# Kernel optimization log

Hardware: AMD Instinct MI355X
Metric: run time of the kernel (lower is better)

## Reference

```python
import jax, jax.numpy as jnp
import numpy as np

BN_EPS = 1e-5
K2 = 9  # 3x3 kernel


def _conv3x3(x, w, b):
    # x: [B,C,H,W], w: [O,C,3,3] -> [B,O,H,W], stride 1, pad 1
    out = jax.lax.conv_general_dilated(
        x, w, window_strides=(1, 1), padding=((1, 1), (1, 1)),
        dimension_numbers=("NCHW", "OIHW", "NCHW"))
    return out + b[None, :, None, None]


def setup_inputs() -> dict:
    key = jax.random.key(0)
    ks = jax.random.split(key, 8)
    B, C, H, W = 8, 256, 64, 64
    O = 256
    x = jax.random.normal(ks[0], (B, C, H, W), dtype=jnp.float32)
    # offset/mask conv: small init so sampled offsets stay near the base grid
    w_off = jax.random.normal(ks[1], (3 * K2, C, 3, 3), dtype=jnp.float32) * 0.01
    b_off = jnp.zeros((3 * K2,), dtype=jnp.float32)
    weight = jax.random.normal(ks[2], (O, C, 3, 3), dtype=jnp.float32) * 0.02
    bias = jnp.zeros((O,), dtype=jnp.float32)
    gamma = jnp.ones((O,), dtype=jnp.float32)
    beta = jnp.zeros((O,), dtype=jnp.float32)
    run_mean = jax.random.normal(ks[3], (O,), dtype=jnp.float32) * 0.1
    run_var = jax.random.uniform(ks[4], (O,), dtype=jnp.float32) + 0.5
    return {"x": x, "w_off": w_off, "b_off": b_off, "weight": weight,
            "bias": bias, "gamma": gamma, "beta": beta,
            "run_mean": run_mean, "run_var": run_var}


def _deform_sample(img, py, px):
    # img: [C,H,W]; py, px: [K2,H,W] sampling coordinates.
    # Bilinear sample with zero padding outside (DCNv2 semantics:
    # out-of-bounds corners contribute zero).
    C, H, W = img.shape
    y0 = jnp.floor(py)
    x0 = jnp.floor(px)
    wy1 = py - y0  # frac weights for the 'high' corner
    wx1 = px - x0

    def gather(yi, xi):
        valid = (yi >= 0) & (yi < H) & (xi >= 0) & (xi < W)
        yc = jnp.clip(yi, 0, H - 1).astype(jnp.int32)
        xc = jnp.clip(xi, 0, W - 1).astype(jnp.int32)
        return img[:, yc, xc] * valid.astype(img.dtype)[None]  # [C,K2,H,W]

    v00 = gather(y0, x0)
    v01 = gather(y0, x0 + 1)
    v10 = gather(y0 + 1, x0)
    v11 = gather(y0 + 1, x0 + 1)
    return (v00 * ((1 - wy1) * (1 - wx1))[None]
            + v01 * ((1 - wy1) * wx1)[None]
            + v10 * (wy1 * (1 - wx1))[None]
            + v11 * (wy1 * wx1)[None])  # [C,K2,H,W]


def reference(x, w_off, b_off, weight, bias, gamma, beta, run_mean, run_var):
    B, C, H, W = x.shape
    O = weight.shape[0]
    # 1) offset / mask branch (standard 3x3 conv)
    om = _conv3x3(x, w_off, b_off)  # [B, 27, H, W]
    off_y = om[:, :K2]
    off_x = om[:, K2:2 * K2]
    mask = jax.nn.sigmoid(om[:, 2 * K2:])  # modulation, [B,9,H,W]
    # 2) base sampling grid for 3x3, stride 1, pad 1, dilation 1
    ky = jnp.repeat(jnp.arange(3), 3).astype(x.dtype)  # [9]
    kx = jnp.tile(jnp.arange(3), 3).astype(x.dtype)    # [9]
    hs = jnp.arange(H, dtype=x.dtype)
    ws = jnp.arange(W, dtype=x.dtype)
    base_y = hs[None, :, None] - 1.0 + ky[:, None, None]  # [9,H,1]
    base_x = ws[None, None, :] - 1.0 + kx[:, None, None]  # [9,1,W]
    py = base_y[None] + off_y  # [B,9,H,W]
    px = base_x[None] + off_x
    # 3) modulated deformable im2col (bilinear gather) per batch
    cols = jax.vmap(_deform_sample)(x, py, px)  # [B,C,9,H,W]
    cols = cols * mask[:, None]                 # apply modulation mask
    # 4) GEMM over (C, K2) + bias
    w3 = weight.reshape(O, C, K2)
    out = jnp.einsum("ock,bckhw->bohw", w3, cols) + bias[None, :, None, None]
    # 5) BatchNorm (eval mode, running stats) + ReLU
    inv = gamma / jnp.sqrt(run_var + BN_EPS)
    out = out * inv[None, :, None, None] + (beta - run_mean * inv)[None, :, None, None]
    return jax.nn.relu(out)
```

## Files before the change

### kernel.cpp

```cpp
#include <hip/hip_runtime.h>
#include <math.h>

#define H 64
#define W 64
#define C 256
#define O 256
#define CK 2304
#define NB 8
#define HWSZ 4096

typedef __attribute__((ext_vector_type(8))) short short8;
typedef __attribute__((ext_vector_type(4))) float floatx4;
typedef __attribute__((ext_vector_type(4))) unsigned uintx4;
typedef __attribute__((ext_vector_type(2))) float f32x2;

#define FSWZ(n) ((((n) & 3) << 1) | (((n) >> 2) & 1))

__device__ __forceinline__ float lo2f(unsigned u) {
  return __builtin_bit_cast(float, u << 16);
}
__device__ __forceinline__ float hi2f(unsigned u) {
  return __builtin_bit_cast(float, u & 0xffff0000u);
}
__device__ __forceinline__ f32x2 up2(unsigned u) {
  return (f32x2){lo2f(u), hi2f(u)};
}
__device__ __forceinline__ unsigned pk2bf(float v0, float v1) {
  unsigned a = __builtin_bit_cast(unsigned, v0);
  unsigned b = __builtin_bit_cast(unsigned, v1);
  return ((a + 0x8000u) >> 16) | ((b + 0x8000u) & 0xffff0000u);
}

__device__ __forceinline__ f32x2 pk_mul(f32x2 a, f32x2 b) {
  f32x2 d;
  asm("v_pk_mul_f32 %0, %1, %2" : "=v"(d) : "v"(a), "v"(b));
  return d;
}
__device__ __forceinline__ f32x2 pk_fma(f32x2 a, f32x2 b, f32x2 c) {
  f32x2 d;
  asm("v_pk_fma_f32 %0, %1, %2, %3" : "=v"(d) : "v"(a), "v"(b), "v"(c));
  return d;
}
__device__ __forceinline__ unsigned cvtpk(f32x2 a) {
  unsigned d;
  asm("v_cvt_pk_bf16_f32 %0, %1, %2" : "=v"(d) : "v"(a[0]), "v"(a[1]));
  return d;
}

__global__ __launch_bounds__(512) void prep_all2(
    const float* __restrict__ x, const float* __restrict__ weight,
    const float* __restrict__ w_off, const float* __restrict__ bias,
    const float* __restrict__ gamma, const float* __restrict__ beta,
    const float* __restrict__ run_mean, const float* __restrict__ run_var,
    unsigned short* __restrict__ xt, unsigned short* __restrict__ wb,
    unsigned short* __restrict__ wob, float* __restrict__ invsh) {
  __shared__ unsigned tile[16384];
  int bid = blockIdx.x;
  int tid = threadIdx.x;

  if (bid < 256) {
    int b = bid >> 5;
    int yg = bid & 31;
    int y0 = yg * 2;
#pragma unroll
    for (int j = 0; j < 4; ++j) {
      int e = tid + 512 * j;
      int xx4 = e & 15;
      int cp = e >> 4;
      const float* p0 = x + ((size_t)b * C + 2 * cp) * HWSZ + y0 * W + xx4 * 4;
      floatx4 f00 = *reinterpret_cast<const floatx4*>(p0);
      floatx4 f01 = *reinterpret_cast<const floatx4*>(p0 + W);
      floatx4 f10 = *reinterpret_cast<const floatx4*>(p0 + HWSZ);
      floatx4 f11 = *reinterpret_cast<const floatx4*>(p0 + HWSZ + W);
      int sw = cp & 31;
#pragma unroll
      for (int k = 0; k < 4; ++k) {
        int px = xx4 * 4 + k;
        tile[cp * 64 + (px ^ sw)] = pk2bf(f00[k], f10[k]);
        tile[8192 + cp * 64 + (px ^ sw)] = pk2bf(f01[k], f11[k]);
      }
    }
    __syncthreads();
    unsigned short* xo = xt + ((size_t)(b * 64 + y0) << 14);
#pragma unroll
    for (int j = 0; j < 8; ++j) {
      int e = tid + 512 * j;
      int cq = e & 31;
      int xx = (e >> 5) & 63;
      int r = e >> 11;
      unsigned u[4];
#pragma unroll
      for (int kk = 0; kk < 4; ++kk) {
        int cpv = cq * 4 + kk;
        u[kk] = tile[r * 8192 + cpv * 64 + (xx ^ (cpv & 31))];
      }
      uint4 v = {u[0], u[1], u[2], u[3]};
      *reinterpret_cast<uint4*>(xo + (r << 14) + (xx << 8) + (cq << 3)) = v;
    }
  } else if (bid < 400) {
    int idx = (bid - 256) * 512 + tid;
    int d0 = idx * 8;
    int lane = idx & 63;
    int mt = (idx >> 6) & 15;
    int ks = idx >> 10;
    int o = mt * 16 + (lane & 15);
    int kn0 = ks * 32 + (lane >> 4) * 8;
    int tap = kn0 >> 8;
    int c0 = kn0 & 255;
    const float* wsrc = weight + o * CK + c0 * 9 + tap;
    unsigned pk[4];
#pragma unroll
    for (int p = 0; p < 4; ++p)
      pk[p] = pk2bf(wsrc[(2 * p) * 9], wsrc[(2 * p + 1) * 9]);
    uint4 v = {pk[0], pk[1], pk[2], pk[3]};
    *reinterpret_cast<uint4*>(wb + d0) = v;
  } else if (bid < 418) {
    int idx = (bid - 400) * 512 + tid;
    int d0 = idx * 8;
    int lane = idx & 63;
    int mt = (idx >> 6) & 1;
    int ks = idx >> 7;
    int o = mt * 16 + (lane & 15);
    int kn0 = ks * 32 + (lane >> 4) * 8;
    int tap = kn0 >> 8;
    int c0 = kn0 & 255;
    uint4 v;
    if (o < 27) {
      const float* wsrc = w_off + o * CK + c0 * 9 + tap;
      unsigned pk[4];
#pragma unroll
      for (int p = 0; p < 4; ++p)
        pk[p] = pk2bf(wsrc[(2 * p) * 9], wsrc[(2 * p + 1) * 9]);
      v = (uint4){pk[0], pk[1], pk[2], pk[3]};
    } else {
      v = (uint4){0, 0, 0, 0};
    }
    *reinterpret_cast<uint4*>(wob + d0) = v;
  } else {
    if (tid < 256) {
      int o = tid;
      float inv = gamma[o] * rsqrtf(run_var[o] + 1e-5f);
      invsh[o] = inv;
      invsh[O + o] = beta[o] + (bias[o] - run_mean[o]) * inv;
    }
  }
}

__global__ __launch_bounds__(512, 2) void deform_mfma_kernel(
    const unsigned short* __restrict__ xt, const unsigned short* __restrict__ wob,
    const float* __restrict__ b_off, const unsigned short* __restrict__ wb,
    const float* __restrict__ invsh, float* __restrict__ out) {
  __shared__ short cols[64 * 256];
  __shared__ float sm_om[27 * 64];
  __shared__ int sbase[576];
  __shared__ float s00[576], s01[576], s10[576], s11[576];

  int tid = threadIdx.x;
  int lane = tid & 63;
  int wvid = tid >> 6;
  int q = lane >> 4;
  int lm = lane & 15;
  int b = blockIdx.x;
  int h = blockIdx.y;
  const unsigned short* xtb = xt + ((size_t)b << 20);

  if (wvid < 4) {
    int mt = wvid & 1;
    int nh = wvid >> 1;
    floatx4 a0[2];
    a0[0] = (floatx4){0.f, 0.f, 0.f, 0.f};
    a0[1] = (floatx4){0.f, 0.f, 0.f, 0.f};
    int pxu[2];
    pxu[0] = (nh * 2 + 0) * 16 + lm;
    pxu[1] = (nh * 2 + 1) * 16 + lm;
    for (int tap = 0; tap < 9; ++tap) {
      int yy = h - 1 + tap / 3;
      bool vy = (yy >= 0) && (yy < H);
      const unsigned short* bp[2];
      bool vv[2];
#pragma unroll
      for (int u = 0; u < 2; ++u) {
        int xx = pxu[u] - 1 + tap % 3;
        vv[u] = vy && (xx >= 0) && (xx < W);
        bp[u] = xtb + ((((yy & 63) << 6) + (xx & 63)) << 8) + q * 8;
      }
#pragma unroll
      for (int s = 0; s < 8; ++s) {
        int ks = tap * 8 + s;
        short8 afrag = *reinterpret_cast<const short8*>(
            wob + (((ks * 2 + mt) * 64 + lane) << 3));
#pragma unroll
        for (int u = 0; u < 2; ++u) {
          short8 bfrag;
          if (vv[u])
            bfrag = *reinterpret_cast<const short8*>(bp[u] + s * 32);
          else
            bfrag = (short8){0, 0, 0, 0, 0, 0, 0, 0};
          a0[u] = __builtin_amdgcn_mfma_f32_16x16x32_bf16(afrag, bfrag, a0[u], 0, 0, 0);
        }
      }
    }
#pragma unroll
    for (int u = 0; u < 2; ++u)
#pragma unroll
      for (int r = 0; r < 4; ++r) {
        int o = mt * 16 + q * 4 + r;
        if (o < 27) sm_om[o * 64 + pxu[u]] = a0[u][r] + b_off[o];
      }
  }
  __syncthreads();

  for (int e = tid; e < 576; e += 512) {
    int n = e & 63;
    int k = e >> 6;
    float oy = sm_om[k * 64 + n];
    float ox = sm_om[(9 + k) * 64 + n];
    float mv = sm_om[(18 + k) * 64 + n];
    float m = 1.0f / (1.0f + __expf(-mv));
    float py = (float)(h - 1 + k / 3) + oy;
    float px = (float)(n - 1 + k % 3) + ox;
    float yf = floorf(py), xf = floorf(px);
    int y0 = (int)yf, x0 = (int)xf;
    float fy = py - yf, fx = px - xf;
    float r0, r1; int yl;
    if (y0 >= 0 && y0 <= H - 2)      { yl = y0;    r0 = 1.f - fy; r1 = fy;       }
    else if (y0 == -1)               { yl = 0;     r0 = fy;       r1 = 0.f;      }
    else if (y0 == H - 1)            { yl = H - 2; r0 = 0.f;      r1 = 1.f - fy; }
    else                             { yl = 0;     r0 = 0.f;      r1 = 0.f;      }
    float c0, c1; int xl;
    if (x0 >= 0 && x0 <= W - 2)      { xl = x0;    c0 = 1.f - fx; c1 = fx;       }
    else if (x0 == -1)               { xl = 0;     c0 = fx;       c1 = 0.f;      }
    else if (x0 == W - 1)            { xl = W - 2; c0 = 0.f;      c1 = 1.f - fx; }
    else                             { xl = 0;     c0 = 0.f;      c1 = 0.f;      }
    r0 *= m; r1 *= m;
    sbase[e] = ((yl << 6) + xl) << 8;
    s00[e] = r0 * c0; s01[e] = r0 * c1;
    s10[e] = r1 * c0; s11[e] = r1 * c1;
  }
  __syncthreads();

  floatx4 acc[2][4];
#pragma unroll
  for (int a = 0; a < 2; ++a)
#pragma unroll
    for (int u = 0; u < 4; ++u) acc[a][u] = (floatx4){0.f, 0.f, 0.f, 0.f};

  int sn = tid >> 3;
  int scb = tid & 7;

  for (int tap = 0; tap < 9; ++tap) {
    if (tap) __syncthreads();
    {
      int ei = tap * 64 + sn;
      int base = sbase[ei];
      float w00 = s00[ei], w01 = s01[ei], w10 = s10[ei], w11 = s11[ei];
      f32x2 W00 = (f32x2){w00, w00};
      f32x2 W01 = (f32x2){w01, w01};
      f32x2 W10 = (f32x2){w10, w10};
      f32x2 W11 = (f32x2){w11, w11};
      const unsigned short* p = xtb + base;
#pragma unroll
      for (int i = 0; i < 4; ++i) {
        int cbw = (i << 3) | scb;
        int co = cbw << 3;
        uintx4 u00 = *reinterpret_cast<const uintx4*>(p + co);
        uintx4 u01 = *reinterpret_cast<const uintx4*>(p + 256 + co);
        uintx4 u10 = *reinterpret_cast<const uintx4*>(p + 16384 + co);
        uintx4 u11 = *reinterpret_cast<const uintx4*>(p + 16640 + co);
        uintx4 res;
#pragma unroll
        for (int jd = 0; jd < 4; ++jd) {
          f32x2 a = pk_mul(up2(u00[jd]), W00);
          a = pk_fma(up2(u01[jd]), W01, a);
          a = pk_fma(up2(u10[jd]), W10, a);
          a = pk_fma(up2(u11[jd]), W11, a);
          res[jd] = cvtpk(a);
        }
        int pos = (cbw ^ FSWZ(sn)) & 31;
        *reinterpret_cast<uintx4*>(&cols[(sn << 8) + (pos << 3)]) = res;
      }
    }
    __syncthreads();

#pragma unroll
    for (int s = 0; s < 8; ++s) {
      int ks = tap * 8 + s;
      short8 afrag[2];
#pragma unroll
      for (int a = 0; a < 2; ++a)
        afrag[a] = *reinterpret_cast<const short8*>(
            wb + (((ks * 16 + wvid * 2 + a) * 64 + lane) << 3));
      short8 bfrag[4];
#pragma unroll
      for (int u = 0; u < 4; ++u) {
        int nn = u * 16 + lm;
        int pos = ((s * 4 + q) ^ FSWZ(nn)) & 31;
        bfrag[u] = *reinterpret_cast<const short8*>(&cols[(nn << 8) + (pos << 3)]);
      }
#pragma unroll
      for (int a = 0; a < 2; ++a)
#pragma unroll
        for (int u = 0; u < 4; ++u)
          acc[a][u] = __builtin_amdgcn_mfma_f32_16x16x32_bf16(
              afrag[a], bfrag[u], acc[a][u], 0, 0, 0);
    }
  }

#pragma unroll
  for (int a = 0; a < 2; ++a) {
#pragma unroll
    for (int u = 0; u < 4; ++u) {
      int nn = u * 16 + lm;
#pragma unroll
      for (int r = 0; r < 4; ++r) {
        int o = (wvid * 2 + a) * 16 + q * 4 + r;
        float v = fmaf(acc[a][u][r], invsh[o], invsh[O + o]);
        out[((size_t)(b * O + o)) * HWSZ + h * W + nn] = fmaxf(v, 0.0f);
      }
    }
  }
}

extern "C" void kernel_launch(void* const* d_in, const int* in_sizes, int n_in,
                              void* d_out, int out_size, void* d_ws, size_t ws_size,
                              hipStream_t stream) {
  const float* x        = (const float*)d_in[0];
  const float* w_off    = (const float*)d_in[1];
  const float* b_off    = (const float*)d_in[2];
  const float* weight   = (const float*)d_in[3];
  const float* bias     = (const float*)d_in[4];
  const float* gamma    = (const float*)d_in[5];
  const float* beta     = (const float*)d_in[6];
  const float* run_mean = (const float*)d_in[7];
  const float* run_var  = (const float*)d_in[8];
  float* out = (float*)d_out;

  char* ws = (char*)d_ws;
  unsigned short* xt = (unsigned short*)ws;
  unsigned short* wbf = (unsigned short*)(ws + 16777216);
  unsigned short* wob = (unsigned short*)(ws + 17956864);
  float* invsh = (float*)(ws + 18104320);

  prep_all2<<<419, 512, 0, stream>>>(x, weight, w_off, bias, gamma, beta,
                                     run_mean, run_var, xt, wbf, wob, invsh);
  {
    dim3 grid(NB, H);
    deform_mfma_kernel<<<grid, 512, 0, stream>>>(xt, wob, b_off, wbf, invsh, out);
  }
}
```

Measured before the change: 186.4 us.

## Process two output rows per block with 1024 threads and per-wave output tiles

Each block now handles two image rows with 1024 threads and a grid half as tall. There are two column buffers, and the offset-conv scratch is aliased onto the column buffer. In the main GEMM each wave owns 16 output channels across 128 pixels, so the weight fragment is loaded once per k-step and reused over 8 MFMAs instead of 2 weight fragments over 4. This is meant to halve weight-fragment global loads per output and improve MFMA-to-load ratio. The cost is higher LDS use per block (about 70KB) and 1024-thread blocks, which may limit occupancy to one block per CU and make barriers costlier.

```diff
diff --git a/kernel.cpp b/kernel.cpp
--- a/kernel.cpp
+++ b/kernel.cpp
@@ -146,14 +146,14 @@
   }
 }
 
-__global__ __launch_bounds__(512, 2) void deform_mfma_kernel(
+__global__ __launch_bounds__(1024, 4) void deform_mfma_kernel(
     const unsigned short* __restrict__ xt, const unsigned short* __restrict__ wob,
     const float* __restrict__ b_off, const unsigned short* __restrict__ wb,
     const float* __restrict__ invsh, float* __restrict__ out) {
-  __shared__ short cols[64 * 256];
-  __shared__ float sm_om[27 * 64];
-  __shared__ int sbase[576];
-  __shared__ float s00[576], s01[576], s10[576], s11[576];
+  __shared__ short cols[2][64 * 256];
+  __shared__ int sbase[1152];
+  __shared__ float s00[1152], s01[1152], s10[1152], s11[1152];
+  float* sm_om = reinterpret_cast<float*>(&cols[0][0]);
 
   int tid = threadIdx.x;
   int lane = tid & 63;
@@ -161,63 +161,53 @@
   int q = lane >> 4;
   int lm = lane & 15;
   int b = blockIdx.x;
-  int h = blockIdx.y;
+  int h0 = blockIdx.y * 2;
   const unsigned short* xtb = xt + ((size_t)b << 20);
 
-  if (wvid < 4) {
+  {
     int mt = wvid & 1;
-    int nh = wvid >> 1;
-    floatx4 a0[2];
-    a0[0] = (floatx4){0.f, 0.f, 0.f, 0.f};
-    a0[1] = (floatx4){0.f, 0.f, 0.f, 0.f};
-    int pxu[2];
-    pxu[0] = (nh * 2 + 0) * 16 + lm;
-    pxu[1] = (nh * 2 + 1) * 16 + lm;
+    int r = (wvid >> 1) & 1;
+    int pxu = wvid >> 2;
+    int px = pxu * 16 + lm;
+    int y = h0 + r;
+    floatx4 a0 = (floatx4){0.f, 0.f, 0.f, 0.f};
     for (int tap = 0; tap < 9; ++tap) {
-      int yy = h - 1 + tap / 3;
-      bool vy = (yy >= 0) && (yy < H);
-      const unsigned short* bp[2];
-      bool vv[2];
-#pragma unroll
-      for (int u = 0; u < 2; ++u) {
-        int xx = pxu[u] - 1 + tap % 3;
-        vv[u] = vy && (xx >= 0) && (xx < W);
-        bp[u] = xtb + ((((yy & 63) << 6) + (xx & 63)) << 8) + q * 8;
-      }
+      int yy = y - 1 + tap / 3;
+      int xx = px - 1 + tap % 3;
+      bool vv = (yy >= 0) && (yy < H) && (xx >= 0) && (xx < W);
+      const unsigned short* bp =
+          xtb + ((((yy & 63) << 6) + (xx & 63)) << 8) + q * 8;
 #pragma unroll
       for (int s = 0; s < 8; ++s) {
         int ks = tap * 8 + s;
         short8 afrag = *reinterpret_cast<const short8*>(
             wob + (((ks * 2 + mt) * 64 + lane) << 3));
-#pragma unroll
-        for (int u = 0; u < 2; ++u) {
-          short8 bfrag;
-          if (vv[u])
-            bfrag = *reinterpret_cast<const short8*>(bp[u] + s * 32);
-          else
-            bfrag = (short8){0, 0, 0, 0, 0, 0, 0, 0};
-          a0[u] = __builtin_amdgcn_mfma_f32_16x16x32_bf16(afrag, bfrag, a0[u], 0, 0, 0);
-        }
-      }
-    }
-#pragma unroll
-    for (int u = 0; u < 2; ++u)
-#pragma unroll
-      for (int r = 0; r < 4; ++r) {
-        int o = mt * 16 + q * 4 + r;
-        if (o < 27) sm_om[o * 64 + pxu[u]] = a0[u][r] + b_off[o];
-      }
+        short8 bfrag;
+        if (vv)
+          bfrag = *reinterpret_cast<const short8*>(bp + s * 32);
+        else
+          bfrag = (short8){0, 0, 0, 0, 0, 0, 0, 0};
+        a0 = __builtin_amdgcn_mfma_f32_16x16x32_bf16(afrag, bfrag, a0, 0, 0, 0);
+      }
+    }
+#pragma unroll
+    for (int rr = 0; rr < 4; ++rr) {
+      int o = mt * 16 + q * 4 + rr;
+      if (o < 27) sm_om[o * 128 + r * 64 + px] = a0[rr] + b_off[o];
+    }
   }
   __syncthreads();
 
-  for (int e = tid; e < 576; e += 512) {
-    int n = e & 63;
-    int k = e >> 6;
-    float oy = sm_om[k * 64 + n];
-    float ox = sm_om[(9 + k) * 64 + n];
-    float mv = sm_om[(18 + k) * 64 + n];
+  for (int e = tid; e < 1152; e += 1024) {
+    int r = (e >= 576) ? 1 : 0;
+    int ei = e - 576 * r;
+    int n = ei & 63;
+    int k = ei >> 6;
+    float oy = sm_om[k * 128 + r * 64 + n];
+    float ox = sm_om[(9 + k) * 128 + r * 64 + n];
+    float mv = sm_om[(18 + k) * 128 + r * 64 + n];
     float m = 1.0f / (1.0f + __expf(-mv));
-    float py = (float)(h - 1 + k / 3) + oy;
+    float py = (float)(h0 + r - 1 + k / 3) + oy;
     float px = (float)(n - 1 + k % 3) + ox;
     float yf = floorf(py), xf = floorf(px);
     int y0 = (int)yf, x0 = (int)xf;
@@ -239,19 +229,19 @@
   }
   __syncthreads();
 
-  floatx4 acc[2][4];
-#pragma unroll
-  for (int a = 0; a < 2; ++a)
-#pragma unroll
-    for (int u = 0; u < 4; ++u) acc[a][u] = (floatx4){0.f, 0.f, 0.f, 0.f};
-
-  int sn = tid >> 3;
+  floatx4 acc[8];
+#pragma unroll
+  for (int u = 0; u < 8; ++u) acc[u] = (floatx4){0.f, 0.f, 0.f, 0.f};
+
+  int snf = tid >> 3;
+  int sr = snf >> 6;
+  int sn = snf & 63;
   int scb = tid & 7;
 
   for (int tap = 0; tap < 9; ++tap) {
     if (tap) __syncthreads();
     {
-      int ei = tap * 64 + sn;
+      int ei = sr * 576 + tap * 64 + sn;
       int base = sbase[ei];
       float w00 = s00[ei], w01 = s01[ei], w10 = s10[ei], w11 = s11[ei];
       f32x2 W00 = (f32x2){w00, w00};
@@ -259,6 +249,7 @@
       f32x2 W10 = (f32x2){w10, w10};
       f32x2 W11 = (f32x2){w11, w11};
       const unsigned short* p = xtb + base;
+      short* colr = &cols[sr][0];
 #pragma unroll
       for (int i = 0; i < 4; ++i) {
         int cbw = (i << 3) | scb;
@@ -277,7 +268,7 @@
           res[jd] = cvtpk(a);
         }
         int pos = (cbw ^ FSWZ(sn)) & 31;
-        *reinterpret_cast<uintx4*>(&cols[(sn << 8) + (pos << 3)]) = res;
+        *reinterpret_cast<uintx4*>(&colr[(sn << 8) + (pos << 3)]) = res;
       }
     }
     __syncthreads();
@@ -285,38 +276,32 @@
 #pragma unroll
     for (int s = 0; s < 8; ++s) {
       int ks = tap * 8 + s;
-      short8 afrag[2];
-#pragma unroll
-      for (int a = 0; a < 2; ++a)
-        afrag[a] = *reinterpret_cast<const short8*>(
-            wb + (((ks * 16 + wvid * 2 + a) * 64 + lane) << 3));
-      short8 bfrag[4];
-#pragma unroll
-      for (int u = 0; u < 4; ++u) {
-        int nn = u * 16 + lm;
+      short8 afrag = *reinterpret_cast<const short8*>(
+          wb + (((ks * 16 + wvid) * 64 + lane) << 3));
+      short8 bfrag[8];
+#pragma unroll
+      for (int u = 0; u < 8; ++u) {
+        int nn = (u & 3) * 16 + lm;
         int pos = ((s * 4 + q) ^ FSWZ(nn)) & 31;
-        bfrag[u] = *reinterpret_cast<const short8*>(&cols[(nn << 8) + (pos << 3)]);
-      }
-#pragma unroll
-      for (int a = 0; a < 2; ++a)
-#pragma unroll
-        for (int u = 0; u < 4; ++u)
-          acc[a][u] = __builtin_amdgcn_mfma_f32_16x16x32_bf16(
-              afrag[a], bfrag[u], acc[a][u], 0, 0, 0);
-    }
-  }
-
-#pragma unroll
-  for (int a = 0; a < 2; ++a) {
-#pragma unroll
-    for (int u = 0; u < 4; ++u) {
-      int nn = u * 16 + lm;
-#pragma unroll
-      for (int r = 0; r < 4; ++r) {
-        int o = (wvid * 2 + a) * 16 + q * 4 + r;
-        float v = fmaf(acc[a][u][r], invsh[o], invsh[O + o]);
-        out[((size_t)(b * O + o)) * HWSZ + h * W + nn] = fmaxf(v, 0.0f);
-      }
+        bfrag[u] = *reinterpret_cast<const short8*>(
+            &cols[u >> 2][(nn << 8) + (pos << 3)]);
+      }
+#pragma unroll
+      for (int u = 0; u < 8; ++u)
+        acc[u] = __builtin_amdgcn_mfma_f32_16x16x32_bf16(
+            afrag, bfrag[u], acc[u], 0, 0, 0);
+    }
+  }
+
+#pragma unroll
+  for (int u = 0; u < 8; ++u) {
+    int r = u >> 2;
+    int nn = (u & 3) * 16 + lm;
+#pragma unroll
+    for (int rr = 0; rr < 4; ++rr) {
+      int o = wvid * 16 + q * 4 + rr;
+      float v = fmaf(acc[u][rr], invsh[o], invsh[O + o]);
+      out[((size_t)(b * O + o)) * HWSZ + (h0 + r) * W + nn] = fmaxf(v, 0.0f);
     }
   }
 }
@@ -344,7 +329,7 @@
   prep_all2<<<419, 512, 0, stream>>>(x, weight, w_off, bias, gamma, beta,
                                      run_mean, run_var, xt, wbf, wob, invsh);
   {
-    dim3 grid(NB, H);
-    deform_mfma_kernel<<<grid, 512, 0, stream>>>(xt, wob, b_off, wbf, invsh, out);
-  }
-}
+    dim3 grid(NB, H / 2);
+    deform_mfma_kernel<<<grid, 1024, 0, stream>>>(xt, wob, b_off, wbf, invsh, out);
+  }
+}
```

New measurement: 201.7 us. 8.2% more time.
